# Kernel tuning notes

Measured on AMD Instinct MI355X. Metric: run time of the kernel, lower is better.

Reference implementation:

```python
import jax, jax.numpy as jnp
import numpy as np

N_GENES = 8192      # input genes
WM = 4              # width_multiplier: hidden nodes per gene
HID = N_GENES * WM  # 32768 hidden units
N_TF = 1024         # embedding dim (TF activities)
GPT = 64            # target genes per TF in the prior network
BATCH = 256
EPS = 1e-5          # BatchNorm1d eps


def _connectivity():
    # layer1: hidden node h belongs to gene h // WM (fan_in = 1)
    rows1 = np.arange(HID, dtype=np.int32)
    cols1 = (rows1 // WM).astype(np.int32)
    # layer2: fully connected within each gene group (WM x WM blocks)
    rows2 = np.repeat(np.arange(HID, dtype=np.int32), WM)
    cols2 = (((np.arange(HID)[:, None] // WM) * WM) + np.arange(WM)).astype(np.int32).ravel()
    # layer3: each TF connects to all WM nodes of GPT randomly chosen genes
    rng = np.random.default_rng(0)
    genes = rng.integers(0, N_GENES, size=(N_TF, GPT))
    cols3 = (genes[:, :, None] * WM + np.arange(WM)).astype(np.int32).reshape(-1)
    rows3 = np.repeat(np.arange(N_TF, dtype=np.int32), GPT * WM)
    return rows1, cols1, rows2, cols2, rows3, cols3


def _sparse_linear(x, w, b, rows, cols, out_dim):
    # y[b, o] = sum_{e: rows[e]==o} w[e] * x[b, cols[e]] + b[o]
    xe = x[:, cols] * w  # [B, E]
    y = jnp.zeros((x.shape[0], out_dim), x.dtype).at[:, rows].add(xe)
    return y + b


def _batchnorm(x):
    # BatchNorm1d(affine=False), training mode: biased batch var
    m = jnp.mean(x, axis=0)
    v = jnp.var(x, axis=0)
    return (x - m) / jnp.sqrt(v + EPS)


def setup_inputs() -> dict:
    key = jax.random.key(0)
    k = jax.random.split(key, 7)
    rows1, cols1, rows2, cols2, rows3, cols3 = _connectivity()
    inp = {
        "features": jax.random.normal(k[0], (BATCH, N_GENES), jnp.float32),
        "w1": jax.random.normal(k[1], (HID,), jnp.float32),                 # fan_in 1
        "b1": jax.random.normal(k[2], (HID,), jnp.float32) * 0.01,
        "w2": jax.random.normal(k[3], (HID * WM,), jnp.float32) / np.sqrt(WM),
        "b2": jax.random.normal(k[4], (HID,), jnp.float32) * 0.01,
        "w3": jax.random.normal(k[5], (N_TF * GPT * WM,), jnp.float32) / np.sqrt(GPT * WM),
        "b3": jax.random.normal(k[6], (N_TF,), jnp.float32) * 0.01,
        "rows1": jnp.asarray(rows1), "cols1": jnp.asarray(cols1),
        "rows2": jnp.asarray(rows2), "cols2": jnp.asarray(cols2),
        "rows3": jnp.asarray(rows3), "cols3": jnp.asarray(cols3),
    }
    return inp


def reference(features, w1, b1, w2, b2, w3, b3,
              rows1, cols1, rows2, cols2, rows3, cols3):
    h = _sparse_linear(features, w1, b1, rows1, cols1, HID)
    h = _batchnorm(jax.nn.relu(h))
    h = _sparse_linear(h, w2, b2, rows2, cols2, HID)
    h = _batchnorm(jax.nn.relu(h))
    z = _sparse_linear(h, w3, b3, rows3, cols3, N_TF)
    return _batchnorm(z)
```

## Files before the change

### kernel.cpp

```cpp
#include <hip/hip_runtime.h>
#include <cstddef>

#define EPS 1e-5f

constexpr int NG  = 8192;
constexpr int HID = 32768;
constexpr int NTF = 1024;
constexpr int B   = 256;

static __device__ __forceinline__ unsigned short f2bf(float v) {
    union { float f; unsigned u; } a; a.f = v;
    unsigned r = a.u + 0x7fffu + ((a.u >> 16) & 1u);
    return (unsigned short)(r >> 16);
}

__global__ __launch_bounds__(256) void fused12(
    const float* __restrict__ x,
    const float* __restrict__ w1,
    const float* __restrict__ b1,
    const float* __restrict__ w2,
    const float* __restrict__ b2,
    unsigned short* __restrict__ h2rT,
    float* __restrict__ m2g,
    float* __restrict__ inv2g)
{
    const int lane  = threadIdx.x & 63;
    const int slice = threadIdx.x >> 6;
    const int c     = (blockIdx.x << 6) + lane;
    const int g     = c >> 2;
    const int b0    = slice << 6;

    __shared__ float redA[4][64], redB[4][64];
    __shared__ float m1s[64], inv1s[64];

    const float w1c = w1[c], b1c = b1[c];
    const float* xp = x + (size_t)b0 * NG + g;

    float s = 0.f, s2 = 0.f;
    #pragma unroll 8
    for (int i = 0; i < 64; ++i) {
        float h = fmaxf(fmaf(w1c, xp[(size_t)i * NG], b1c), 0.f);
        s += h;
        s2 = fmaf(h, h, s2);
    }
    redA[slice][lane] = s;
    redB[slice][lane] = s2;
    __syncthreads();
    if (slice == 0) {
        float S  = redA[0][lane] + redA[1][lane] + redA[2][lane] + redA[3][lane];
        float S2 = redB[0][lane] + redB[1][lane] + redB[2][lane] + redB[3][lane];
        float m  = S * (1.f / 256.f);
        float v  = fmaf(-m, m, S2 * (1.f / 256.f));
        m1s[lane]   = m;
        inv1s[lane] = rsqrtf(v + EPS);
    }
    __syncthreads();

    const int lbase = lane & ~3;
    const int gbase = g << 2;
    float w1j[4], b1j[4], w2s[4];
    float bconst = b2[c];
    #pragma unroll
    for (int j = 0; j < 4; ++j) {
        w1j[j] = w1[gbase + j];
        b1j[j] = b1[gbase + j];
        float wv = w2[(c << 2) + j] * inv1s[lbase + j];
        w2s[j] = wv;
        bconst = fmaf(-wv, m1s[lbase + j], bconst);
    }

    float t2s = 0.f, t2s2 = 0.f;
    unsigned short* op = h2rT + (size_t)c * B + b0;
    for (int i0 = 0; i0 < 64; i0 += 4) {
        ushort4 pk;
        unsigned short* pp = (unsigned short*)&pk;
        #pragma unroll
        for (int u = 0; u < 4; ++u) {
            float v = xp[(size_t)(i0 + u) * NG];
            float acc = bconst;
            #pragma unroll
            for (int j = 0; j < 4; ++j) {
                float r = fmaxf(fmaf(w1j[j], v, b1j[j]), 0.f);
                acc = fmaf(w2s[j], r, acc);
            }
            float r2 = fmaxf(acc, 0.f);
            t2s += r2;
            t2s2 = fmaf(r2, r2, t2s2);
            pp[u] = f2bf(r2);
        }
        *(ushort4*)(op + i0) = pk;
    }

    __syncthreads();
    redA[slice][lane] = t2s;
    redB[slice][lane] = t2s2;
    __syncthreads();
    if (slice == 0) {
        float S  = redA[0][lane] + redA[1][lane] + redA[2][lane] + redA[3][lane];
        float S2 = redB[0][lane] + redB[1][lane] + redB[2][lane] + redB[3][lane];
        float m  = S * (1.f / 256.f);
        float v  = fmaf(-m, m, S2 * (1.f / 256.f));
        m2g[c]   = m;
        inv2g[c] = rsqrtf(v + EPS);
    }
}

__global__ __launch_bounds__(256) void fused3(
    const unsigned short* __restrict__ h2,
    const float* __restrict__ m2g,
    const float* __restrict__ inv2g,
    const float* __restrict__ w3,
    const float* __restrict__ b3,
    const int*   __restrict__ cols3,
    float* __restrict__ out)
{
    const int t   = blockIdx.x;
    const int tid = threadIdx.x;

    __shared__ float wls[256];
    __shared__ int   als[256];
    __shared__ float wred[4], rs[4], rs2[4];
    __shared__ float acc01[2][256];

    int   col = cols3[(t << 8) + tid];
    float wv  = w3[(t << 8) + tid] * inv2g[col];
    wls[tid]  = wv;
    als[tid]  = col << 8;
    float bp  = wv * m2g[col];
    #pragma unroll
    for (int o = 32; o > 0; o >>= 1) bp += __shfl_xor(bp, o);
    if ((tid & 63) == 0) wred[tid >> 6] = bp;
    __syncthreads();

    const int half = tid >> 7;
    const int r2   = (tid & 127) << 1;
    float a0 = 0.f, a1 = 0.f;
    #pragma unroll 8
    for (int e2 = 0; e2 < 128; ++e2) {
        const int e = (e2 << 1) + half;
        float w = wls[e];
        unsigned u = *(const unsigned*)(h2 + als[e] + r2);
        union { unsigned u; float f; } lo, hi;
        lo.u = u << 16;
        hi.u = u & 0xffff0000u;
        a0 = fmaf(w, lo.f, a0);
        a1 = fmaf(w, hi.f, a1);
    }
    *(float2*)&acc01[half][r2] = make_float2(a0, a1);
    __syncthreads();

    const float zbias = b3[t] - (wred[0] + wred[1] + wred[2] + wred[3]);
    float z = acc01[0][tid] + acc01[1][tid] + zbias;

    float s = z, s2 = z * z;
    #pragma unroll
    for (int o = 32; o > 0; o >>= 1) {
        s  += __shfl_xor(s, o);
        s2 += __shfl_xor(s2, o);
    }
    if ((tid & 63) == 0) { rs[tid >> 6] = s; rs2[tid >> 6] = s2; }
    __syncthreads();
    float S  = rs[0] + rs[1] + rs[2] + rs[3];
    float S2 = rs2[0] + rs2[1] + rs2[2] + rs2[3];
    float m  = S * (1.f / 256.f);
    float v  = fmaf(-m, m, S2 * (1.f / 256.f));
    float invs = rsqrtf(v + EPS);
    out[(size_t)tid * NTF + t] = (z - m) * invs;
}

extern "C" void kernel_launch(void* const* d_in, const int* in_sizes, int n_in,
                              void* d_out, int out_size, void* d_ws, size_t ws_size,
                              hipStream_t stream) {
    const float* x   = (const float*)d_in[0];
    const float* w1  = (const float*)d_in[1];
    const float* b1  = (const float*)d_in[2];
    const float* w2  = (const float*)d_in[3];
    const float* b2  = (const float*)d_in[4];
    const float* w3  = (const float*)d_in[5];
    const float* b3  = (const float*)d_in[6];
    const int* cols3 = (const int*)d_in[12];
    float* out = (float*)d_out;

    unsigned short* h2rT = (unsigned short*)d_ws;
    float* m2g   = (float*)(h2rT + (size_t)HID * B);
    float* inv2g = m2g + HID;

    fused12<<<HID / 64, 256, 0, stream>>>(x, w1, b1, w2, b2, h2rT, m2g, inv2g);
    fused3<<<NTF, 256, 0, stream>>>(h2rT, m2g, inv2g, w3, b3, cols3, out);
}
```

Baseline: 117.9 us.

## Split layer-3 gather into prep, batch-sliced gather, and BN kernels

Replaces the single fused3 kernel (one block per TF) with three kernels. prep3 folds inv2g into w3 and precomputes byte offsets. gather3 runs 8 blocks per TF, each covering 32 batch rows, so the gather is spread over more blocks. bn3 then applies the final batchnorm. The constant bias and mean terms are dropped because batchnorm cancels them, and this also removes the m2g output. The price is two extra launches and a zraw round trip through global memory.

```diff
diff --git a/kernel.cpp b/kernel.cpp
--- a/kernel.cpp
+++ b/kernel.cpp
@@ -21,7 +21,6 @@
     const float* __restrict__ w2,
     const float* __restrict__ b2,
     unsigned short* __restrict__ h2rT,
-    float* __restrict__ m2g,
     float* __restrict__ inv2g)
 {
     const int lane  = threadIdx.x & 63;
@@ -100,58 +99,79 @@
         float S2 = redB[0][lane] + redB[1][lane] + redB[2][lane] + redB[3][lane];
         float m  = S * (1.f / 256.f);
         float v  = fmaf(-m, m, S2 * (1.f / 256.f));
-        m2g[c]   = m;
         inv2g[c] = rsqrtf(v + EPS);
     }
 }
 
-__global__ __launch_bounds__(256) void fused3(
+__global__ __launch_bounds__(256) void prep3(
+    const float* __restrict__ w3,
+    const int*   __restrict__ cols3,
+    const float* __restrict__ inv2g,
+    float* __restrict__ wfold,
+    int*   __restrict__ colb)
+{
+    const int i = (blockIdx.x << 8) + threadIdx.x;
+    const int col = cols3[i];
+    wfold[i] = w3[i] * inv2g[col];
+    colb[i]  = col << 9;
+}
+
+__global__ __launch_bounds__(256) void gather3(
     const unsigned short* __restrict__ h2,
-    const float* __restrict__ m2g,
-    const float* __restrict__ inv2g,
-    const float* __restrict__ w3,
-    const float* __restrict__ b3,
-    const int*   __restrict__ cols3,
+    const float* __restrict__ wfold,
+    const int*   __restrict__ colb,
+    float* __restrict__ zraw)
+{
+    const int slice = blockIdx.x & 7;
+    const int t     = blockIdx.x >> 3;
+    const int tid   = threadIdx.x;
+
+    __shared__ float wls[256];
+    __shared__ int   alds[256];
+    __shared__ float sred[16][33];
+
+    wls[tid]  = wfold[(t << 8) + tid];
+    alds[tid] = colb[(t << 8) + tid];
+    __syncthreads();
+
+    const int eg = tid >> 4;
+    const int r2 = tid & 15;
+    const int boff = (slice << 6) + (r2 << 2);
+    const char* h2c = (const char*)h2;
+
+    float a0 = 0.f, a1 = 0.f;
+    #pragma unroll
+    for (int k = 0; k < 16; ++k) {
+        const int e = (k << 4) | eg;
+        float w = wls[e];
+        unsigned u = *(const unsigned*)(h2c + alds[e] + boff);
+        union { unsigned v; float f; } lo, hi;
+        lo.v = u << 16;
+        hi.v = u & 0xffff0000u;
+        a0 = fmaf(w, lo.f, a0);
+        a1 = fmaf(w, hi.f, a1);
+    }
+    sred[eg][(r2 << 1)]     = a0;
+    sred[eg][(r2 << 1) + 1] = a1;
+    __syncthreads();
+
+    if (tid < 32) {
+        float s = 0.f;
+        #pragma unroll
+        for (int e = 0; e < 16; ++e) s += sred[e][tid];
+        zraw[(t << 8) + (slice << 5) + tid] = s;
+    }
+}
+
+__global__ __launch_bounds__(256) void bn3(
+    const float* __restrict__ zraw,
     float* __restrict__ out)
 {
     const int t   = blockIdx.x;
     const int tid = threadIdx.x;
-
-    __shared__ float wls[256];
-    __shared__ int   als[256];
-    __shared__ float wred[4], rs[4], rs2[4];
-    __shared__ float acc01[2][256];
-
-    int   col = cols3[(t << 8) + tid];
-    float wv  = w3[(t << 8) + tid] * inv2g[col];
-    wls[tid]  = wv;
-    als[tid]  = col << 8;
-    float bp  = wv * m2g[col];
-    #pragma unroll
-    for (int o = 32; o > 0; o >>= 1) bp += __shfl_xor(bp, o);
-    if ((tid & 63) == 0) wred[tid >> 6] = bp;
-    __syncthreads();
-
-    const int half = tid >> 7;
-    const int r2   = (tid & 127) << 1;
-    float a0 = 0.f, a1 = 0.f;
-    #pragma unroll 8
-    for (int e2 = 0; e2 < 128; ++e2) {
-        const int e = (e2 << 1) + half;
-        float w = wls[e];
-        unsigned u = *(const unsigned*)(h2 + als[e] + r2);
-        union { unsigned u; float f; } lo, hi;
-        lo.u = u << 16;
-        hi.u = u & 0xffff0000u;
-        a0 = fmaf(w, lo.f, a0);
-        a1 = fmaf(w, hi.f, a1);
-    }
-    *(float2*)&acc01[half][r2] = make_float2(a0, a1);
-    __syncthreads();
-
-    const float zbias = b3[t] - (wred[0] + wred[1] + wred[2] + wred[3]);
-    float z = acc01[0][tid] + acc01[1][tid] + zbias;
-
+    __shared__ float rs[4], rs2[4];
+
+    float z = zraw[(t << 8) + tid];
     float s = z, s2 = z * z;
     #pragma unroll
     for (int o = 32; o > 0; o >>= 1) {
@@ -164,8 +184,7 @@
     float S2 = rs2[0] + rs2[1] + rs2[2] + rs2[3];
     float m  = S * (1.f / 256.f);
     float v  = fmaf(-m, m, S2 * (1.f / 256.f));
-    float invs = rsqrtf(v + EPS);
-    out[(size_t)tid * NTF + t] = (z - m) * invs;
+    out[(size_t)tid * NTF + t] = (z - m) * rsqrtf(v + EPS);
 }
 
 extern "C" void kernel_launch(void* const* d_in, const int* in_sizes, int n_in,
@@ -177,14 +196,18 @@
     const float* w2  = (const float*)d_in[3];
     const float* b2  = (const float*)d_in[4];
     const float* w3  = (const float*)d_in[5];
-    const float* b3  = (const float*)d_in[6];
+    const float* b3  = (const float*)d_in[6];  (void)b3;
     const int* cols3 = (const int*)d_in[12];
     float* out = (float*)d_out;
 
     unsigned short* h2rT = (unsigned short*)d_ws;
-    float* m2g   = (float*)(h2rT + (size_t)HID * B);
-    float* inv2g = m2g + HID;
-
-    fused12<<<HID / 64, 256, 0, stream>>>(x, w1, b1, w2, b2, h2rT, m2g, inv2g);
-    fused3<<<NTF, 256, 0, stream>>>(h2rT, m2g, inv2g, w3, b3, cols3, out);
-}
+    float* inv2g = (float*)(h2rT + (size_t)HID * B);
+    float* wfold = inv2g + HID;
+    int*   colb  = (int*)(wfold + NTF * 256);
+    float* zraw  = (float*)(colb + NTF * 256);
+
+    fused12<<<HID / 64, 256, 0, stream>>>(x, w1, b1, w2, b2, h2rT, inv2g);
+    prep3  <<<NTF,      256, 0, stream>>>(w3, cols3, inv2g, wfold, colb);
+    gather3<<<NTF * 8,  256, 0, stream>>>(h2rT, wfold, colb, zraw);
+    bn3    <<<NTF,      256, 0, stream>>>(zraw, out);
+}
```

After: 121.9 us. +3.3%, slower.
